# Kernel optimization log

Measured on AMD Instinct MI355X. Metric: run time of the kernel, lower is better.

The kernel has to match this reference:

```python
import jax, jax.numpy as jnp
import numpy as np

H = 16  # number of heads

def setup_inputs() -> dict:
    key = jax.random.key(0)
    ks = jax.random.split(key, 9)
    B, N, D = 2, 2048, 1024
    s = 0.02
    q = jax.random.normal(ks[0], (B, N, D), jnp.float32)
    k = jax.random.normal(ks[1], (B, N, D), jnp.float32)
    v = jax.random.normal(ks[2], (B, N, D), jnp.float32)
    mask = jax.random.randint(ks[3], (B, 1, N, N), 0, 2).astype(bool)
    Wq = jax.random.normal(ks[4], (D, D), jnp.float32) * s
    Wk = jax.random.normal(ks[5], (D, D), jnp.float32) * s
    Wv = jax.random.normal(ks[6], (D, D), jnp.float32) * s
    Wo = jax.random.normal(ks[7], (D, D), jnp.float32) * s
    bq = jnp.zeros((D,), jnp.float32)
    bk = jnp.zeros((D,), jnp.float32)
    bv = jnp.zeros((D,), jnp.float32)
    bo = jnp.zeros((D,), jnp.float32)
    return {"q": q, "k": k, "v": v, "mask": mask,
            "Wq": Wq, "bq": bq, "Wk": Wk, "bk": bk,
            "Wv": Wv, "bv": bv, "Wo": Wo, "bo": bo}


def reference(q, k, v, mask, Wq, bq, Wk, bk, Wv, bv, Wo, bo):
    B, N, D = q.shape
    dk = D // H
    # nn.Linear: x @ W.T + b, then split heads: b n (h d) -> b h n d
    def proj(x, W, b):
        return (x @ W.T + b).reshape(B, N, H, dk).transpose(0, 2, 1, 3)
    qh = proj(q, Wq, bq)  # [B,H,N,dk]
    kh = proj(k, Wk, bk)
    vh = proj(v, Wv, bv)
    # NOTE: original has NO 1/sqrt(dk) scaling
    score = jnp.einsum('bhnd,bhmd->bhnm', qh, kh)
    score = jnp.where(mask, jnp.float32(-1e9), score)
    attn = jax.nn.softmax(score, axis=-1)
    x = jnp.einsum('bhnm,bhmd->bhnd', attn, vh)
    x = x.transpose(0, 2, 1, 3).reshape(B, N, D)  # b h n d -> b n (h d)
    return x @ Wo.T + bo
```

## Files before the change

kernel.cpp:

```cpp
#include <hip/hip_runtime.h>
#include <math.h>

#define BB 2
#define NN 2048
#define DD 1024
#define HH 16
#define DK 64
#define LOG2E 1.4426950408889634f

typedef __attribute__((ext_vector_type(8))) short short8;
typedef __attribute__((ext_vector_type(4))) float f32x4;
typedef __attribute__((ext_vector_type(16))) float f32x16;
typedef __attribute__((ext_vector_type(4))) float f32x4v;
typedef __attribute__((ext_vector_type(8))) unsigned short ushort8;
typedef unsigned long long u64;

__device__ __forceinline__ unsigned short f2bf(float f) {
  unsigned u = __float_as_uint(f);
  unsigned r = (u + 0x7FFFu + ((u >> 16) & 1u)) >> 16;
  return (unsigned short)r;
}

__device__ __forceinline__ void gload_lds16(const void* g, void* l) {
  auto gp = (const __attribute__((address_space(1))) unsigned int*)(unsigned long long)g;
  auto lp = (__attribute__((address_space(3))) unsigned int*)(unsigned int)(unsigned long long)l;
  __builtin_amdgcn_global_load_lds(gp, lp, 16, 0, 0);
}

__global__ __launch_bounds__(256) void cvt_all(
    const float* __restrict__ q, const float* __restrict__ k, const float* __restrict__ v,
    const float* __restrict__ wq, const float* __restrict__ wk, const float* __restrict__ wv,
    const float* __restrict__ wo, unsigned short* __restrict__ ws)
{
  const long NW = (long)DD * DD;
  const long NX = (long)BB * NN * DD;
  long i = ((long)blockIdx.x * blockDim.x + threadIdx.x) * 8;
  if (i >= 4 * NW + 3 * NX) return;
  const float* src; unsigned short* dst; long off;
  if (i < 4 * NW) {
    int s = (int)(i / NW);
    src = (s == 0) ? wq : (s == 1) ? wk : (s == 2) ? wv : wo;
    off = i - (long)s * NW;
    dst = ws + (long)s * NW + off;
  } else {
    long j = i - 4 * NW;
    int s = (int)(j / NX);
    src = (s == 0) ? q : (s == 1) ? k : v;
    off = j - (long)s * NX;
    dst = ws + 4 * NW + (long)s * NX + off;
  }
  f32x4v a = *(const f32x4v*)(src + off);
  f32x4v b = *(const f32x4v*)(src + off + 4);
  ushort8 o;
  o[0] = f2bf(a[0]); o[1] = f2bf(a[1]); o[2] = f2bf(a[2]); o[3] = f2bf(a[3]);
  o[4] = f2bf(b[0]); o[5] = f2bf(b[1]); o[6] = f2bf(b[2]); o[7] = f2bf(b[3]);
  *(ushort8*)dst = o;
}

__global__ __launch_bounds__(256) void cvt_mask_bits(const void* __restrict__ mask,
                                                     u64* __restrict__ mb, long total64)
{
  const unsigned char* m8 = (const unsigned char*)mask;
  const int l = threadIdx.x & 63;
  unsigned probe = m8[l * 4 + 1] | m8[l * 4 + 2] | m8[l * 4 + 3];
  const bool isBool = (__any(probe != 0) != 0);

  long t = (long)blockIdx.x * blockDim.x + threadIdx.x;
  if (t >= total64) return;
  u64 bits = 0;
  if (isBool) {
    const uint4* p = (const uint4*)(m8 + t * 64);
#pragma unroll
    for (int i = 0; i < 4; ++i) {
      uint4 q4 = p[i];
      unsigned vv[4] = {q4.x, q4.y, q4.z, q4.w};
#pragma unroll
      for (int j = 0; j < 4; ++j)
#pragma unroll
        for (int bb = 0; bb < 4; ++bb)
          bits |= (u64)((vv[j] >> (8 * bb)) & 1u) << (i * 16 + j * 4 + bb);
    }
  } else {
    const int4* p = (const int4*)((const int*)mask + t * 64);
#pragma unroll
    for (int i = 0; i < 16; ++i) {
      int4 q4 = p[i];
      bits |= (u64)(q4.x & 1) << (i * 4);
      bits |= (u64)(q4.y & 1) << (i * 4 + 1);
      bits |= (u64)(q4.z & 1) << (i * 4 + 2);
      bits |= (u64)(q4.w & 1) << (i * 4 + 3);
    }
  }
  const long bb2 = t >> 16;
  const long qq = (t >> 5) & 2047;
  const long tcol = t & 31;
  mb[(bb2 * 32 + tcol) * 2048 + qq] = bits;
}

struct GemmArgs {
  const unsigned short* A;
  const unsigned short* Bw;
  const float* bias;
  void* C;
  int mode;
  float oscale;
};

template<int TM, int BN>
__global__ __launch_bounds__(256) void gemm_bt(GemmArgs ga0, GemmArgs ga1, GemmArgs ga2)
{
  constexpr int K = DD;
  constexpr int Nn = DD;
  constexpr int GX = 1024 / BN;
  constexpr int GY = 4096 / TM;
  constexpr int PERZ = GX * GY;
  constexpr int MF = TM / 32;
  constexpr int NF = BN / 32;
  constexpr int NT = K / 32;
  constexpr int LPS = TM / 64 + BN / 64;
  __shared__ __align__(16) unsigned short As[3][TM * 32];
  __shared__ __align__(16) unsigned short Bs[3][BN * 32];

  int wgid = blockIdx.x + (blockIdx.y + blockIdx.z * GY) * GX;
  const int nwg = (int)gridDim.z * PERZ;
  const int chunk = nwg >> 3;
  wgid = (wgid & 7) * chunk + (wgid >> 3);
  const int zi = wgid / PERZ;
  const int rem = wgid % PERZ;
  const int m0 = (rem / GX) * TM;
  const int n0 = (rem % GX) * BN;
  GemmArgs ga = (zi == 0) ? ga0 : ((zi == 1) ? ga1 : ga2);

  const int tid = threadIdx.x;
  const int lane = tid & 63;
  const int w = tid >> 6;
  const int m_woff = (w >> 1) * (TM / 2);
  const int n_woff = (w & 1) * (BN / 2);
  const int c = lane & 15, g = lane >> 4;

  f32x4 acc[MF][NF];
  const f32x4 z4 = {0.f, 0.f, 0.f, 0.f};
#pragma unroll
  for (int m = 0; m < MF; ++m)
#pragma unroll
    for (int n = 0; n < NF; ++n) acc[m][n] = z4;

  const unsigned short* Ab = ga.A + (long)m0 * K;
  const unsigned short* Bb = ga.Bw + (long)n0 * K;
  const int ar = tid >> 2;
  const int ac = ((tid & 3) ^ (ar & 3)) * 8;

  auto STAGE = [&](int buf, int kk) {
#pragma unroll
    for (int i = 0; i < TM / 64; ++i)
      gload_lds16(Ab + (long)(i * 64 + ar) * K + kk + ac, &As[buf][i * 2048 + tid * 8]);
#pragma unroll
    for (int i = 0; i < BN / 64; ++i)
      gload_lds16(Bb + (long)(i * 64 + ar) * K + kk + ac, &Bs[buf][i * 2048 + tid * 8]);
  };

  STAGE(0, 0);
  STAGE(1, 32);

  const int rswz = (g ^ (c & 3)) * 8;

  for (int t = 0; t < NT; ++t) {
    if (t < NT - 1) {
      if constexpr (LPS == 4)
        asm volatile("s_waitcnt vmcnt(4)" ::: "memory");
      else
        asm volatile("s_waitcnt vmcnt(3)" ::: "memory");
    } else {
      asm volatile("s_waitcnt vmcnt(0)" ::: "memory");
    }
    __builtin_amdgcn_s_barrier();
    __builtin_amdgcn_sched_barrier(0);
    if (t + 2 < NT) STAGE((t + 2) % 3, (t + 2) * 32);

    const int cb = t % 3;
    short8 a[MF], b[NF];
#pragma unroll
    for (int m = 0; m < MF; ++m)
      a[m] = *(const short8*)&As[cb][(m_woff + 16 * m + c) * 32 + rswz];
#pragma unroll
    for (int n = 0; n < NF; ++n)
      b[n] = *(const short8*)&Bs[cb][(n_woff + 16 * n + c) * 32 + rswz];
    __builtin_amdgcn_s_setprio(1);
#pragma unroll
    for (int m = 0; m < MF; ++m)
#pragma unroll
      for (int n = 0; n < NF; ++n)
        acc[m][n] = __builtin_amdgcn_mfma_f32_16x16x32_bf16(a[m], b[n], acc[m][n], 0, 0, 0);
    __builtin_amdgcn_s_setprio(0);
  }

#pragma unroll
  for (int n = 0; n < NF; ++n) {
    const int col = n0 + n_woff + 16 * n + c;
    const float bv = ga.bias[col];
#pragma unroll
    for (int m = 0; m < MF; ++m) {
      const int row0 = m0 + m_woff + 16 * m + 4 * g;
#pragma unroll
      for (int r = 0; r < 4; ++r) {
        const int row = row0 + r;
        const float val = (acc[m][n][r] + bv) * ga.oscale;
        if (ga.mode == 1)
          ((float*)ga.C)[(long)row * Nn + col] = val;
        else if (ga.mode == 0)
          ((unsigned short*)ga.C)[(long)row * Nn + col] = f2bf(val);
        else
          ((unsigned short*)ga.C)[((long)(row >> 11) * DD + col) * NN + (row & (NN - 1))] = f2bf(val);
      }
    }
  }
}

__global__ __launch_bounds__(256, 2) void attn_kernel(
    const unsigned short* __restrict__ Q,
    const unsigned short* __restrict__ K,
    const unsigned short* __restrict__ Vt,
    const u64* __restrict__ mb64,
    unsigned short* __restrict__ ctx)
{
  __shared__ __align__(16) unsigned short Ks[2][64 * 64];
  __shared__ __align__(16) unsigned short Vs[2][64 * 64];

  const int tid = threadIdx.x;
  const int lane = tid & 63;
  const int w = tid >> 6;
  const int bid = blockIdx.x;
  const int b = (bid >> 4) & 1, h = bid & 15;
  const int q0 = (bid >> 5) * 128;
  const int l31 = lane & 31;
  const int hi = lane >> 5;
  const int qrow = q0 + 32 * w + l31;

  short8 aq[4];
  {
    const unsigned short* qp = Q + ((long)(b * NN + qrow)) * DD + h * DK + 8 * hi;
    aq[0] = *(const short8*)(qp);
    aq[1] = *(const short8*)(qp + 16);
    aq[2] = *(const short8*)(qp + 32);
    aq[3] = *(const short8*)(qp + 48);
  }

  f32x16 o0, o1, cinit;
#pragma unroll
  for (int r = 0; r < 16; ++r) { o0[r] = 0.f; o1[r] = 0.f; cinit[r] = -28.853901f; }
  float lsum = 0.f;

  const unsigned short* Kbase = K + (long)(b * NN) * DD + h * DK;
  const unsigned short* Vbase = Vt + ((long)(b * DD + h * DK)) * NN;
  const u64* mbase = mb64 + (long)(b * 32) * 2048 + qrow;

  const int srow = tid >> 3;
  const int scol = tid & 7;
  const int swcol = scol ^ (srow & 7);

  auto STAGE = [&](int buf, int t) {
#pragma unroll
    for (int hf = 0; hf < 2; ++hf) {
      const int row = srow + 32 * hf;
      gload_lds16(Kbase + (long)(t * 64 + row) * DD + swcol * 8, &Ks[buf][hf * 2048 + tid * 8]);
      gload_lds16(Vbase + (long)row * NN + t * 64 + swcol * 8, &Vs[buf][hf * 2048 + tid * 8]);
    }
  };

  STAGE(0, 0);
  __syncthreads();
  int cur = 0;
  const int sh4 = 4 * hi;
  u64 mword = mbase[0];

  for (int t = 0; t < 32; ++t) {
    const u64 mnext = (t < 31) ? mbase[(long)(t + 1) * 2048] : 0;
    if (t < 31) STAGE(cur ^ 1, t + 1);
    const unsigned msk0 = ((unsigned)mword) >> sh4;
    const unsigned msk1 = ((unsigned)(mword >> 32)) >> sh4;

#pragma unroll
    for (int sub = 0; sub < 2; ++sub) {
      const unsigned m = sub ? msk1 : msk0;
      const int krow = l31 + 32 * sub;
      const int kswz = (krow & 7) << 3;

      f32x16 ss = cinit;
      __builtin_amdgcn_s_setprio(1);
#pragma unroll
      for (int i = 0; i < 4; ++i) {
        const short8 kf = *(const short8*)&Ks[cur][krow * 64 + ((16 * i + 8 * hi) ^ kswz)];
        ss = __builtin_amdgcn_mfma_f32_32x32x16_bf16(kf, aq[i], ss, 0, 0, 0);
      }
      __builtin_amdgcn_s_setprio(0);

      float p[16];
#pragma unroll
      for (int r = 0; r < 16; ++r) {
        const int cr = (r & 3) + 8 * (r >> 2);
        const float e = ((m >> cr) & 1u) ? -1e9f : ss[r];
        p[r] = __builtin_amdgcn_exp2f(e);
        lsum += p[r];
      }

      unsigned wv[8];
#pragma unroll
      for (int i = 0; i < 8; ++i) {
        unsigned rr;
        asm("v_cvt_pk_bf16_f32 %0, %1, %2" : "=v"(rr) : "v"(p[2 * i]), "v"(p[2 * i + 1]));
        wv[i] = rr;
      }
      asm("v_permlane32_swap_b32 %0, %1" : "+v"(wv[0]), "+v"(wv[2]));
      asm("v_permlane32_swap_b32 %0, %1" : "+v"(wv[1]), "+v"(wv[3]));
      asm("v_permlane32_swap_b32 %0, %1" : "+v"(wv[4]), "+v"(wv[6]));
      asm("v_permlane32_swap_b32 %0, %1" : "+v"(wv[5]), "+v"(wv[7]));
      union { short8 s; unsigned u[4]; } pa0, pa1;
      pa0.u[0] = wv[0]; pa0.u[1] = wv[1]; pa0.u[2] = wv[2]; pa0.u[3] = wv[3];
      pa1.u[0] = wv[4]; pa1.u[1] = wv[5]; pa1.u[2] = wv[6]; pa1.u[3] = wv[7];

      __builtin_amdgcn_s_setprio(1);
#pragma unroll
      for (int dblk = 0; dblk < 2; ++dblk) {
        const int vrow = l31 + 32 * dblk;
        const int vswz = (vrow & 7) << 3;
        const short8 vb0 = *(const short8*)&Vs[cur][vrow * 64 + ((32 * sub + 8 * hi) ^ vswz)];
        const short8 vb1 = *(const short8*)&Vs[cur][vrow * 64 + ((32 * sub + 16 + 8 * hi) ^ vswz)];
        if (dblk == 0) {
          o0 = __builtin_amdgcn_mfma_f32_32x32x16_bf16(pa0.s, vb0, o0, 0, 0, 0);
          o0 = __builtin_amdgcn_mfma_f32_32x32x16_bf16(pa1.s, vb1, o0, 0, 0, 0);
        } else {
          o1 = __builtin_amdgcn_mfma_f32_32x32x16_bf16(pa0.s, vb0, o1, 0, 0, 0);
          o1 = __builtin_amdgcn_mfma_f32_32x32x16_bf16(pa1.s, vb1, o1, 0, 0, 0);
        }
      }
      __builtin_amdgcn_s_setprio(0);
    }
    __syncthreads();
    cur ^= 1;
    mword = mnext;
  }

  lsum += __shfl_xor(lsum, 32);
  const float inv = 1.0f / lsum;

#pragma unroll
  for (int r = 0; r < 16; ++r) {
    const int qr = (r & 3) + 8 * (r >> 2) + 4 * hi;
    const float linv = __shfl(inv, qr);
    const long row = (long)(b * NN + q0 + 32 * w + qr);
    ctx[row * DD + h * DK + l31] = f2bf(o0[r] * linv);
    ctx[row * DD + h * DK + 32 + l31] = f2bf(o1[r] * linv);
  }
}

extern "C" void kernel_launch(void* const* d_in, const int* in_sizes, int n_in,
                              void* d_out, int out_size, void* d_ws, size_t ws_size,
                              hipStream_t stream) {
  const float* q  = (const float*)d_in[0];
  const float* k  = (const float*)d_in[1];
  const float* v  = (const float*)d_in[2];
  const void*  mask = d_in[3];
  const float* Wq = (const float*)d_in[4];
  const float* bq = (const float*)d_in[5];
  const float* Wk = (const float*)d_in[6];
  const float* bk = (const float*)d_in[7];
  const float* Wv = (const float*)d_in[8];
  const float* bv = (const float*)d_in[9];
  const float* Wo = (const float*)d_in[10];
  const float* bo = (const float*)d_in[11];

  unsigned short* ws = (unsigned short*)d_ws;
  const long NW = (long)DD * DD;
  const long NX = (long)BB * NN * DD;
  unsigned short* Wqb = ws;
  unsigned short* Wkb = ws + NW;
  unsigned short* Wvb = ws + 2 * NW;
  unsigned short* Wob = ws + 3 * NW;
  unsigned short* Xq  = ws + 4 * NW;
  unsigned short* Xk  = Xq + NX;
  unsigned short* Xv  = Xk + NX;
  unsigned short* Qh  = Xv + NX;
  unsigned short* Kh  = Qh + NX;
  unsigned short* Vtr = Kh + NX;
  unsigned short* Ctx = Vtr + NX;
  u64* Mbits = (u64*)(Ctx + NX);
  const long NM64 = (long)BB * NN * NN / 64;

  cvt_all<<<8192, 256, 0, stream>>>(q, k, v, Wq, Wk, Wv, Wo, ws);
  cvt_mask_bits<<<(int)(NM64 / 256), 256, 0, stream>>>(mask, Mbits, NM64);

  GemmArgs gq = {Xq, Wqb, bq, (void*)Qh, 0, LOG2E};
  GemmArgs gk = {Xk, Wkb, bk, (void*)Kh, 0, 1.0f};
  GemmArgs gv = {Xv, Wvb, bv, (void*)Vtr, 2, 1.0f};
  dim3 gproj(DD / 128, (BB * NN) / 128, 3);
  gemm_bt<128, 128><<<gproj, 256, 0, stream>>>(gq, gk, gv);

  attn_kernel<<<512, 256, 0, stream>>>(Qh, Kh, Vtr, Mbits, Ctx);

  GemmArgs go = {Ctx, Wob, bo, d_out, 1, 1.0f};
  dim3 gout(DD / 128, (BB * NN) / 64, 1);
  gemm_bt<64, 128><<<gout, 256, 0, stream>>>(go, go, go);
}
```

Baseline: 143.9 us.

## Fuse fp32-to-bf16 activation conversion into projection GEMM A-tile loading

The projection GEMM now reads fp32 q/k/v directly into registers, converts them to bf16 with packed cvt instructions, and writes them into swizzled LDS one stage ahead. This removes the separate conversion pass over the activations and its bf16 intermediate buffers. The attention kernel also precomputes its LDS offsets and splits the row-sum accumulator into two. The fused path trades async global-to-LDS loads for register-staged loads, which raises register pressure and adds VALU work inside the GEMM main loop.

```diff
diff --git a/kernel.cpp b/kernel.cpp
--- a/kernel.cpp
+++ b/kernel.cpp
@@ -21,34 +21,29 @@
   return (unsigned short)r;
 }
 
+__device__ __forceinline__ unsigned cvtpk(float a, float b) {
+  unsigned r;
+  asm("v_cvt_pk_bf16_f32 %0, %1, %2" : "=v"(r) : "v"(a), "v"(b));
+  return r;
+}
+
 __device__ __forceinline__ void gload_lds16(const void* g, void* l) {
   auto gp = (const __attribute__((address_space(1))) unsigned int*)(unsigned long long)g;
   auto lp = (__attribute__((address_space(3))) unsigned int*)(unsigned int)(unsigned long long)l;
   __builtin_amdgcn_global_load_lds(gp, lp, 16, 0, 0);
 }
 
-__global__ __launch_bounds__(256) void cvt_all(
-    const float* __restrict__ q, const float* __restrict__ k, const float* __restrict__ v,
+__global__ __launch_bounds__(256) void cvt_w(
     const float* __restrict__ wq, const float* __restrict__ wk, const float* __restrict__ wv,
     const float* __restrict__ wo, unsigned short* __restrict__ ws)
 {
   const long NW = (long)DD * DD;
-  const long NX = (long)BB * NN * DD;
   long i = ((long)blockIdx.x * blockDim.x + threadIdx.x) * 8;
-  if (i >= 4 * NW + 3 * NX) return;
-  const float* src; unsigned short* dst; long off;
-  if (i < 4 * NW) {
-    int s = (int)(i / NW);
-    src = (s == 0) ? wq : (s == 1) ? wk : (s == 2) ? wv : wo;
-    off = i - (long)s * NW;
-    dst = ws + (long)s * NW + off;
-  } else {
-    long j = i - 4 * NW;
-    int s = (int)(j / NX);
-    src = (s == 0) ? q : (s == 1) ? k : v;
-    off = j - (long)s * NX;
-    dst = ws + 4 * NW + (long)s * NX + off;
-  }
+  if (i >= 4 * NW) return;
+  int s = (int)(i / NW);
+  const float* src = (s == 0) ? wq : (s == 1) ? wk : (s == 2) ? wv : wo;
+  long off = i - (long)s * NW;
+  unsigned short* dst = ws + (long)s * NW + off;
   f32x4v a = *(const f32x4v*)(src + off);
   f32x4v b = *(const f32x4v*)(src + off + 4);
   ushort8 o;
@@ -98,7 +93,7 @@
 }
 
 struct GemmArgs {
-  const unsigned short* A;
+  const void* A;
   const unsigned short* Bw;
   const float* bias;
   void* C;
@@ -106,7 +101,7 @@
   float oscale;
 };
 
-template<int TM, int BN>
+template<int TM, int BN, int AFP32>
 __global__ __launch_bounds__(256) void gemm_bt(GemmArgs ga0, GemmArgs ga1, GemmArgs ga2)
 {
   constexpr int K = DD;
@@ -117,7 +112,6 @@
   constexpr int MF = TM / 32;
   constexpr int NF = BN / 32;
   constexpr int NT = K / 32;
-  constexpr int LPS = TM / 64 + BN / 64;
   __shared__ __align__(16) unsigned short As[3][TM * 32];
   __shared__ __align__(16) unsigned short Bs[3][BN * 32];
 
@@ -145,37 +139,80 @@
 #pragma unroll
     for (int n = 0; n < NF; ++n) acc[m][n] = z4;
 
-  const unsigned short* Ab = ga.A + (long)m0 * K;
   const unsigned short* Bb = ga.Bw + (long)n0 * K;
   const int ar = tid >> 2;
   const int ac = ((tid & 3) ^ (ar & 3)) * 8;
 
-  auto STAGE = [&](int buf, int kk) {
-#pragma unroll
-    for (int i = 0; i < TM / 64; ++i)
-      gload_lds16(Ab + (long)(i * 64 + ar) * K + kk + ac, &As[buf][i * 2048 + tid * 8]);
+  auto STAGE_B = [&](int buf, int kk) {
 #pragma unroll
     for (int i = 0; i < BN / 64; ++i)
       gload_lds16(Bb + (long)(i * 64 + ar) * K + kk + ac, &Bs[buf][i * 2048 + tid * 8]);
   };
 
-  STAGE(0, 0);
-  STAGE(1, 32);
+  const unsigned short* Ab16 = (const unsigned short*)ga.A + (long)m0 * K;
+  const int arow = tid >> 1;
+  const int ahalf = tid & 1;
+  const float* Afp = (const float*)ga.A + (long)(m0 + arow) * K + ahalf * 16;
+  f32x4v areg[4];
+
+  auto STAGE_A16 = [&](int buf, int kk) {
+#pragma unroll
+    for (int i = 0; i < TM / 64; ++i)
+      gload_lds16(Ab16 + (long)(i * 64 + ar) * K + kk + ac, &As[buf][i * 2048 + tid * 8]);
+  };
+  auto LOAD_A = [&](int kk) {
+#pragma unroll
+    for (int j = 0; j < 4; ++j) areg[j] = *(const f32x4v*)(Afp + kk + 4 * j);
+  };
+  auto WRITE_A = [&](int buf) {
+    union { short8 s; unsigned u[4]; } p0, p1;
+#pragma unroll
+    for (int k = 0; k < 4; ++k) p0.u[k] = cvtpk(areg[k >> 1][(k & 1) * 2], areg[k >> 1][(k & 1) * 2 + 1]);
+#pragma unroll
+    for (int k = 0; k < 4; ++k) p1.u[k] = cvtpk(areg[(k + 4) >> 1][(k & 1) * 2], areg[(k + 4) >> 1][(k & 1) * 2 + 1]);
+    const int G0 = (2 * ahalf) ^ (arow & 3);
+    const int G1 = (2 * ahalf + 1) ^ (arow & 3);
+    *(short8*)((char*)&As[buf][0] + arow * 64 + G0 * 16) = p0.s;
+    *(short8*)((char*)&As[buf][0] + arow * 64 + G1 * 16) = p1.s;
+  };
+
+  if constexpr (AFP32) {
+    LOAD_A(0);
+    STAGE_B(0, 0);
+    WRITE_A(0);
+    LOAD_A(32);
+    STAGE_B(1, 32);
+  } else {
+    STAGE_A16(0, 0);
+    STAGE_B(0, 0);
+    STAGE_A16(1, 32);
+    STAGE_B(1, 32);
+  }
 
   const int rswz = (g ^ (c & 3)) * 8;
 
   for (int t = 0; t < NT; ++t) {
-    if (t < NT - 1) {
-      if constexpr (LPS == 4)
-        asm volatile("s_waitcnt vmcnt(4)" ::: "memory");
-      else
-        asm volatile("s_waitcnt vmcnt(3)" ::: "memory");
+    if constexpr (AFP32) {
+      if (t < NT - 1) asm volatile("s_waitcnt vmcnt(2)" ::: "memory");
+      else            asm volatile("s_waitcnt vmcnt(0)" ::: "memory");
     } else {
-      asm volatile("s_waitcnt vmcnt(0)" ::: "memory");
+      constexpr int LPS = TM / 64 + BN / 64;
+      if (t < NT - 1) {
+        if constexpr (LPS == 4) asm volatile("s_waitcnt vmcnt(4)" ::: "memory");
+        else                    asm volatile("s_waitcnt vmcnt(3)" ::: "memory");
+      } else {
+        asm volatile("s_waitcnt vmcnt(0)" ::: "memory");
+      }
     }
     __builtin_amdgcn_s_barrier();
     __builtin_amdgcn_sched_barrier(0);
-    if (t + 2 < NT) STAGE((t + 2) % 3, (t + 2) * 32);
+
+    if constexpr (AFP32) {
+      if (t + 1 < NT) WRITE_A((t + 1) % 3);
+      if (t + 2 < NT) { LOAD_A((t + 2) * 32); STAGE_B((t + 2) % 3, (t + 2) * 32); }
+    } else {
+      if (t + 2 < NT) { STAGE_A16((t + 2) % 3, (t + 2) * 32); STAGE_B((t + 2) % 3, (t + 2) * 32); }
+    }
 
     const int cb = t % 3;
     short8 a[MF], b[NF];
@@ -248,7 +285,7 @@
   f32x16 o0, o1, cinit;
 #pragma unroll
   for (int r = 0; r < 16; ++r) { o0[r] = 0.f; o1[r] = 0.f; cinit[r] = -28.853901f; }
-  float lsum = 0.f;
+  float ls0 = 0.f, ls1 = 0.f;
 
   const unsigned short* Kbase = K + (long)(b * NN) * DD + h * DK;
   const unsigned short* Vbase = Vt + ((long)(b * DD + h * DK)) * NN;
@@ -266,6 +303,22 @@
       gload_lds16(Vbase + (long)row * NN + t * 64 + swcol * 8, &Vs[buf][hf * 2048 + tid * 8]);
     }
   };
+
+  int koffs[8], voff0[4], voff1[4];
+#pragma unroll
+  for (int sub = 0; sub < 2; ++sub) {
+    const int krow = l31 + 32 * sub;
+    const int kswz = (l31 & 7) << 3;
+#pragma unroll
+    for (int i = 0; i < 4; ++i)
+      koffs[sub * 4 + i] = krow * 64 + ((16 * i + 8 * hi) ^ kswz);
+#pragma unroll
+    for (int dblk = 0; dblk < 2; ++dblk) {
+      const int vrow = l31 + 32 * dblk;
+      voff0[sub * 2 + dblk] = vrow * 64 + ((32 * sub + 8 * hi) ^ kswz);
+      voff1[sub * 2 + dblk] = vrow * 64 + ((32 * sub + 16 + 8 * hi) ^ kswz);
+    }
+  }
 
   STAGE(0, 0);
   __syncthreads();
@@ -282,34 +335,30 @@
 #pragma unroll
     for (int sub = 0; sub < 2; ++sub) {
       const unsigned m = sub ? msk1 : msk0;
-      const int krow = l31 + 32 * sub;
-      const int kswz = (krow & 7) << 3;
 
       f32x16 ss = cinit;
       __builtin_amdgcn_s_setprio(1);
 #pragma unroll
       for (int i = 0; i < 4; ++i) {
-        const short8 kf = *(const short8*)&Ks[cur][krow * 64 + ((16 * i + 8 * hi) ^ kswz)];
+        const short8 kf = *(const short8*)&Ks[cur][koffs[sub * 4 + i]];
         ss = __builtin_amdgcn_mfma_f32_32x32x16_bf16(kf, aq[i], ss, 0, 0, 0);
       }
       __builtin_amdgcn_s_setprio(0);
 
       float p[16];
+      float lacc = 0.f;
 #pragma unroll
       for (int r = 0; r < 16; ++r) {
         const int cr = (r & 3) + 8 * (r >> 2);
         const float e = ((m >> cr) & 1u) ? -1e9f : ss[r];
         p[r] = __builtin_amdgcn_exp2f(e);
-        lsum += p[r];
+        lacc += p[r];
       }
+      if (sub == 0) ls0 += lacc; else ls1 += lacc;
 
       unsigned wv[8];
 #pragma unroll
-      for (int i = 0; i < 8; ++i) {
-        unsigned rr;
-        asm("v_cvt_pk_bf16_f32 %0, %1, %2" : "=v"(rr) : "v"(p[2 * i]), "v"(p[2 * i + 1]));
-        wv[i] = rr;
-      }
+      for (int i = 0; i < 8; ++i) wv[i] = cvtpk(p[2 * i], p[2 * i + 1]);
       asm("v_permlane32_swap_b32 %0, %1" : "+v"(wv[0]), "+v"(wv[2]));
       asm("v_permlane32_swap_b32 %0, %1" : "+v"(wv[1]), "+v"(wv[3]));
       asm("v_permlane32_swap_b32 %0, %1" : "+v"(wv[4]), "+v"(wv[6]));
@@ -319,19 +368,15 @@
       pa1.u[0] = wv[4]; pa1.u[1] = wv[5]; pa1.u[2] = wv[6]; pa1.u[3] = wv[7];
 
       __builtin_amdgcn_s_setprio(1);
-#pragma unroll
-      for (int dblk = 0; dblk < 2; ++dblk) {
-        const int vrow = l31 + 32 * dblk;
-        const int vswz = (vrow & 7) << 3;
-        const short8 vb0 = *(const short8*)&Vs[cur][vrow * 64 + ((32 * sub + 8 * hi) ^ vswz)];
-        const short8 vb1 = *(const short8*)&Vs[cur][vrow * 64 + ((32 * sub + 16 + 8 * hi) ^ vswz)];
-        if (dblk == 0) {
-          o0 = __builtin_amdgcn_mfma_f32_32x32x16_bf16(pa0.s, vb0, o0, 0, 0, 0);
-          o0 = __builtin_amdgcn_mfma_f32_32x32x16_bf16(pa1.s, vb1, o0, 0, 0, 0);
-        } else {
-          o1 = __builtin_amdgcn_mfma_f32_32x32x16_bf16(pa0.s, vb0, o1, 0, 0, 0);
-          o1 = __builtin_amdgcn_mfma_f32_32x32x16_bf16(pa1.s, vb1, o1, 0, 0, 0);
-        }
+      {
+        const short8 vb00 = *(const short8*)&Vs[cur][voff0[sub * 2 + 0]];
+        const short8 vb10 = *(const short8*)&Vs[cur][voff1[sub * 2 + 0]];
+        o0 = __builtin_amdgcn_mfma_f32_32x32x16_bf16(pa0.s, vb00, o0, 0, 0, 0);
+        o0 = __builtin_amdgcn_mfma_f32_32x32x16_bf16(pa1.s, vb10, o0, 0, 0, 0);
+        const short8 vb01 = *(const short8*)&Vs[cur][voff0[sub * 2 + 1]];
+        const short8 vb11 = *(const short8*)&Vs[cur][voff1[sub * 2 + 1]];
+        o1 = __builtin_amdgcn_mfma_f32_32x32x16_bf16(pa0.s, vb01, o1, 0, 0, 0);
+        o1 = __builtin_amdgcn_mfma_f32_32x32x16_bf16(pa1.s, vb11, o1, 0, 0, 0);
       }
       __builtin_amdgcn_s_setprio(0);
     }
@@ -340,6 +385,7 @@
     mword = mnext;
   }
 
+  float lsum = ls0 + ls1;
   lsum += __shfl_xor(lsum, 32);
   const float inv = 1.0f / lsum;
 
@@ -376,28 +422,25 @@
   unsigned short* Wkb = ws + NW;
   unsigned short* Wvb = ws + 2 * NW;
   unsigned short* Wob = ws + 3 * NW;
-  unsigned short* Xq  = ws + 4 * NW;
-  unsigned short* Xk  = Xq + NX;
-  unsigned short* Xv  = Xk + NX;
-  unsigned short* Qh  = Xv + NX;
+  unsigned short* Qh  = ws + 4 * NW;
   unsigned short* Kh  = Qh + NX;
   unsigned short* Vtr = Kh + NX;
   unsigned short* Ctx = Vtr + NX;
   u64* Mbits = (u64*)(Ctx + NX);
   const long NM64 = (long)BB * NN * NN / 64;
 
-  cvt_all<<<8192, 256, 0, stream>>>(q, k, v, Wq, Wk, Wv, Wo, ws);
+  cvt_w<<<2048, 256, 0, stream>>>(Wq, Wk, Wv, Wo, ws);
   cvt_mask_bits<<<(int)(NM64 / 256), 256, 0, stream>>>(mask, Mbits, NM64);
 
-  GemmArgs gq = {Xq, Wqb, bq, (void*)Qh, 0, LOG2E};
-  GemmArgs gk = {Xk, Wkb, bk, (void*)Kh, 0, 1.0f};
-  GemmArgs gv = {Xv, Wvb, bv, (void*)Vtr, 2, 1.0f};
+  GemmArgs gq = {q, Wqb, bq, (void*)Qh, 0, LOG2E};
+  GemmArgs gk = {k, Wkb, bk, (void*)Kh, 0, 1.0f};
+  GemmArgs gv = {v, Wvb, bv, (void*)Vtr, 2, 1.0f};
   dim3 gproj(DD / 128, (BB * NN) / 128, 3);
-  gemm_bt<128, 128><<<gproj, 256, 0, stream>>>(gq, gk, gv);
+  gemm_bt<128, 128, 1><<<gproj, 256, 0, stream>>>(gq, gk, gv);
 
   attn_kernel<<<512, 256, 0, stream>>>(Qh, Kh, Vtr, Mbits, Ctx);
 
   GemmArgs go = {Ctx, Wob, bo, d_out, 1, 1.0f};
   dim3 gout(DD / 128, (BB * NN) / 64, 1);
-  gemm_bt<64, 128><<<gout, 256, 0, stream>>>(go, go, go);
-}
+  gemm_bt<64, 128, 0><<<gout, 256, 0, stream>>>(go, go, go);
+}
```

After: 141.8 us. About the same (-1.5%).
